# Performance work log

Hardware: AMD Instinct MI355X
Metric: run time of the kernel (lower is better)

The kernel has to match this reference:

```python
import jax, jax.numpy as jnp
import numpy as np

N = 100000   # nodes
K = 32       # fixed neighbor count per node
IN_C = 128
OUT_C = 64


def setup_inputs() -> dict:
    key = jax.random.key(0)
    k1, k2, k3 = jax.random.split(key, 3)
    x = jax.random.normal(k1, (N, IN_C), dtype=jnp.float32)
    nbrs = jax.random.randint(k2, (N, K), 0, N, dtype=jnp.int64)
    # nn.Linear weight [out, in], no bias
    W = jax.random.normal(k3, (OUT_C, IN_C), dtype=jnp.float32) * (1.0 / np.sqrt(IN_C))
    return {"x": x, "nbrs": nbrs, "W": W}


def reference(x, nbrs, W):
    # h = self.w(x): [N, out]
    h = jnp.einsum("ni,oi->no", x, W)
    # gather neighbor features: [N, K, out]
    gathered = h[nbrs]
    # torch.median(dim=0): lower middle element of sorted values (no averaging)
    med_idx = (K - 1) // 2
    out = jnp.sort(gathered, axis=1)[:, med_idx, :]  # [N, out]
    return out
```

## Files before the change

### kernel.cpp

```cpp
#include <hip/hip_runtime.h>
#include <hip/hip_fp16.h>

#define NNODES 100000
#define KNBR 32
#define IN_C 128
#define OUT_C 64

__global__ __launch_bounds__(256) void gemm_h_kernel(
    const float* __restrict__ x, const float* __restrict__ W,
    __half* __restrict__ h)
{
    __shared__ __align__(16) float sx[64 * 68];
    __shared__ __align__(16) float sw[64 * 68];

    const int t = threadIdx.x;
    const int node0 = blockIdx.x * 64;
    const int tx = t & 15;
    const int ty = t >> 4;
    const int kq = t & 15;
    const int sl = t >> 4;

    float acc[4][4];
#pragma unroll
    for (int i = 0; i < 4; ++i)
#pragma unroll
        for (int j = 0; j < 4; ++j) acc[i][j] = 0.f;

    for (int kc = 0; kc < 2; ++kc) {
        const int kbase = kc * 64;
        __syncthreads();
#pragma unroll
        for (int pass = 0; pass < 4; ++pass) {
            const int nl = sl + pass * 16;
            int nn = node0 + nl;
            if (nn > NNODES - 1) nn = NNODES - 1;
            const float4 xv = *(const float4*)(x + nn * IN_C + kbase + 4 * kq);
            sx[(4 * kq + 0) * 68 + nl] = xv.x;
            sx[(4 * kq + 1) * 68 + nl] = xv.y;
            sx[(4 * kq + 2) * 68 + nl] = xv.z;
            sx[(4 * kq + 3) * 68 + nl] = xv.w;
            const float4 wv = *(const float4*)(W + nl * IN_C + kbase + 4 * kq);
            sw[(4 * kq + 0) * 68 + nl] = wv.x;
            sw[(4 * kq + 1) * 68 + nl] = wv.y;
            sw[(4 * kq + 2) * 68 + nl] = wv.z;
            sw[(4 * kq + 3) * 68 + nl] = wv.w;
        }
        __syncthreads();
#pragma unroll 8
        for (int kk = 0; kk < 64; ++kk) {
            const float4 wv = *(const float4*)&sw[kk * 68 + 4 * tx];
            const float4 xv = *(const float4*)&sx[kk * 68 + 4 * ty];
            acc[0][0] += xv.x * wv.x; acc[0][1] += xv.x * wv.y;
            acc[0][2] += xv.x * wv.z; acc[0][3] += xv.x * wv.w;
            acc[1][0] += xv.y * wv.x; acc[1][1] += xv.y * wv.y;
            acc[1][2] += xv.y * wv.z; acc[1][3] += xv.y * wv.w;
            acc[2][0] += xv.z * wv.x; acc[2][1] += xv.z * wv.y;
            acc[2][2] += xv.z * wv.z; acc[2][3] += xv.z * wv.w;
            acc[3][0] += xv.w * wv.x; acc[3][1] += xv.w * wv.y;
            acc[3][2] += xv.w * wv.z; acc[3][3] += xv.w * wv.w;
        }
    }
#pragma unroll
    for (int i = 0; i < 4; ++i) {
        const int node = node0 + 4 * ty + i;
        if (node < NNODES) {
            __half2 p0 = __floats2half2_rn(acc[i][0], acc[i][1]);
            __half2 p1 = __floats2half2_rn(acc[i][2], acc[i][3]);
            uint2 st;
            st.x = *(unsigned int*)&p0;
            st.y = *(unsigned int*)&p1;
            *(uint2*)(h + node * OUT_C + 4 * tx) = st;
        }
    }
}

__device__ __forceinline__ unsigned pk_min(unsigned a, unsigned b) {
    unsigned d;
    asm("v_pk_min_f16 %0, %1, %2" : "=v"(d) : "v"(a), "v"(b));
    return d;
}
__device__ __forceinline__ unsigned pk_max(unsigned a, unsigned b) {
    unsigned d;
    asm("v_pk_max_f16 %0, %1, %2" : "=v"(d) : "v"(a), "v"(b));
    return d;
}
__device__ __forceinline__ void ce(unsigned& a, unsigned& b) {
    const unsigned lo = pk_min(a, b);
    b = pk_max(a, b);
    a = lo;
}

__device__ __forceinline__ void sort16(unsigned* v) {
    constexpr unsigned char net[63][2] = {
        {0,1},{2,3},{4,5},{6,7},{8,9},{10,11},{12,13},{14,15},
        {0,2},{1,3},{4,6},{5,7},{8,10},{9,11},{12,14},{13,15},
        {1,2},{5,6},{9,10},{13,14},
        {0,4},{1,5},{2,6},{3,7},{8,12},{9,13},{10,14},{11,15},
        {2,4},{3,5},{10,12},{11,13},
        {1,2},{3,4},{5,6},{9,10},{11,12},{13,14},
        {0,8},{1,9},{2,10},{3,11},{4,12},{5,13},{6,14},{7,15},
        {4,8},{5,9},{6,10},{7,11},
        {2,4},{3,5},{6,8},{7,9},{10,12},{11,13},
        {1,2},{3,4},{5,6},{7,8},{9,10},{11,12},{13,14}
    };
#pragma unroll
    for (int i = 0; i < 63; ++i) ce(v[net[i][0]], v[net[i][1]]);
}

__device__ __forceinline__ unsigned median32(unsigned* v) {
    sort16(v);
    sort16(v + 16);
    const unsigned* A = v;
    const unsigned* B = v + 16;
    const unsigned e2a = pk_max(pk_max(A[0], B[0]), pk_min(A[8],  B[8]));
    const unsigned o1a = pk_min(pk_max(A[4], B[4]), pk_min(A[12], B[12]));
    const unsigned Ep4 = pk_max(e2a, o1a);
    const unsigned e2b = pk_max(pk_max(A[2], B[2]), pk_min(A[10], B[10]));
    const unsigned o1b = pk_min(pk_max(A[6], B[6]), pk_min(A[14], B[14]));
    const unsigned Op3 = pk_min(e2b, o1b);
    const unsigned E8  = pk_max(Ep4, Op3);
    const unsigned e2c = pk_max(pk_max(A[1], B[1]), pk_min(A[9],  B[9]));
    const unsigned o1c = pk_min(pk_max(A[5], B[5]), pk_min(A[13], B[13]));
    const unsigned Ep4o = pk_max(e2c, o1c);
    const unsigned e2d = pk_max(pk_max(A[3], B[3]), pk_min(A[11], B[11]));
    const unsigned o1d = pk_min(pk_max(A[7], B[7]), pk_min(A[15], B[15]));
    const unsigned Op3o = pk_min(e2d, o1d);
    const unsigned O7  = pk_min(Ep4o, Op3o);
    return pk_min(E8, O7);
}

__global__ __launch_bounds__(256) void median_kernel(
    const __half* __restrict__ h, const int* __restrict__ nbrs,
    float* __restrict__ out)
{
    const int t = threadIdx.x;
    const int li = t & 15;
    const int node = blockIdx.x * 16 + (t >> 4);
    const int ch0 = 4 * li;

    const int ia = nbrs[node * KNBR + li];
    const int ib = nbrs[node * KNBR + 16 + li];

    unsigned a[KNBR];
    unsigned b[KNBR];
#pragma unroll
    for (int k = 0; k < KNBR; ++k) {
        const int row = (k < 16) ? __shfl(ia, k, 16) : __shfl(ib, k - 16, 16);
        const uint2 rv = *(const uint2*)(h + row * OUT_C + ch0);
        a[k] = rv.x;
        b[k] = rv.y;
    }

    const unsigned ma = median32(a);
    const unsigned mb = median32(b);
    const __half2 ha = *(const __half2*)&ma;
    const __half2 hb = *(const __half2*)&mb;

    float4 o;
    o.x = __low2float(ha);
    o.y = __high2float(ha);
    o.z = __low2float(hb);
    o.w = __high2float(hb);
    *(float4*)(out + node * OUT_C + ch0) = o;
}

extern "C" void kernel_launch(void* const* d_in, const int* in_sizes, int n_in,
                              void* d_out, int out_size, void* d_ws, size_t ws_size,
                              hipStream_t stream) {
    (void)in_sizes; (void)n_in; (void)out_size; (void)ws_size;
    const float* x    = (const float*)d_in[0];
    const int*   nbrs = (const int*)d_in[1];
    const float* W    = (const float*)d_in[2];
    float* out = (float*)d_out;
    __half* h  = (__half*)d_ws;

    gemm_h_kernel<<<(NNODES + 63) / 64, 256, 0, stream>>>(x, W, h);
    median_kernel<<<NNODES / 16, 256, 0, stream>>>(h, nbrs, out);
}
```

Measured before the change: 163.3 us.

## Use fp16 MFMA for projection GEMM and nontemporal access in median kernel

Replaces the shared-memory fp32 FMA GEMM with a one-wavefront-per-16-node kernel that converts x and W to fp16 in registers and uses 16x16x32 f16 MFMA instructions, with no LDS staging or barriers. Each block reloads and converts the full W into register fragments. Neighbor indices are loaded and outputs stored with nontemporal hints so streaming data does not displace the gathered h rows in cache. Rounding x and W to fp16 with round-toward-zero before accumulating adds precision loss, and the output stores from the MFMA layout are scalar half writes.

```diff
diff --git a/kernel.cpp b/kernel.cpp
--- a/kernel.cpp
+++ b/kernel.cpp
@@ -5,73 +5,55 @@
 #define KNBR 32
 #define IN_C 128
 #define OUT_C 64
+#define NTILES (NNODES / 16)
 
-__global__ __launch_bounds__(256) void gemm_h_kernel(
+typedef _Float16 half8  __attribute__((ext_vector_type(8)));
+typedef __fp16   fp16x2 __attribute__((ext_vector_type(2)));
+typedef float    f4     __attribute__((ext_vector_type(4)));
+
+union H8 { half8 v; fp16x2 h2[4]; };
+
+__device__ __forceinline__ half8 load_frag_f32(const float* p) {
+    const float4 a = *(const float4*)p;
+    const float4 b = *(const float4*)(p + 4);
+    H8 r;
+    r.h2[0] = __builtin_amdgcn_cvt_pkrtz(a.x, a.y);
+    r.h2[1] = __builtin_amdgcn_cvt_pkrtz(a.z, a.w);
+    r.h2[2] = __builtin_amdgcn_cvt_pkrtz(b.x, b.y);
+    r.h2[3] = __builtin_amdgcn_cvt_pkrtz(b.z, b.w);
+    return r.v;
+}
+
+__global__ __launch_bounds__(64) void gemm_h_kernel(
     const float* __restrict__ x, const float* __restrict__ W,
     __half* __restrict__ h)
 {
-    __shared__ __align__(16) float sx[64 * 68];
-    __shared__ __align__(16) float sw[64 * 68];
+    const int l = threadIdx.x;
+    const int m = l & 15;
+    const int q = l >> 4;
+    const int node0 = blockIdx.x * 16;
 
-    const int t = threadIdx.x;
-    const int node0 = blockIdx.x * 64;
-    const int tx = t & 15;
-    const int ty = t >> 4;
-    const int kq = t & 15;
-    const int sl = t >> 4;
+    half8 wf[4][4];
+#pragma unroll
+    for (int b = 0; b < 4; ++b)
+#pragma unroll
+        for (int kc = 0; kc < 4; ++kc)
+            wf[b][kc] = load_frag_f32(W + (16 * b + m) * IN_C + kc * 32 + 8 * q);
 
-    float acc[4][4];
+    f4 acc[4] = {};
 #pragma unroll
-    for (int i = 0; i < 4; ++i)
+    for (int kc = 0; kc < 4; ++kc) {
+        const half8 af = load_frag_f32(x + (size_t)(node0 + m) * IN_C + kc * 32 + 8 * q);
 #pragma unroll
-        for (int j = 0; j < 4; ++j) acc[i][j] = 0.f;
+        for (int b = 0; b < 4; ++b)
+            acc[b] = __builtin_amdgcn_mfma_f32_16x16x32_f16(af, wf[b][kc], acc[b], 0, 0, 0);
+    }
 
-    for (int kc = 0; kc < 2; ++kc) {
-        const int kbase = kc * 64;
-        __syncthreads();
 #pragma unroll
-        for (int pass = 0; pass < 4; ++pass) {
-            const int nl = sl + pass * 16;
-            int nn = node0 + nl;
-            if (nn > NNODES - 1) nn = NNODES - 1;
-            const float4 xv = *(const float4*)(x + nn * IN_C + kbase + 4 * kq);
-            sx[(4 * kq + 0) * 68 + nl] = xv.x;
-            sx[(4 * kq + 1) * 68 + nl] = xv.y;
-            sx[(4 * kq + 2) * 68 + nl] = xv.z;
-            sx[(4 * kq + 3) * 68 + nl] = xv.w;
-            const float4 wv = *(const float4*)(W + nl * IN_C + kbase + 4 * kq);
-            sw[(4 * kq + 0) * 68 + nl] = wv.x;
-            sw[(4 * kq + 1) * 68 + nl] = wv.y;
-            sw[(4 * kq + 2) * 68 + nl] = wv.z;
-            sw[(4 * kq + 3) * 68 + nl] = wv.w;
-        }
-        __syncthreads();
-#pragma unroll 8
-        for (int kk = 0; kk < 64; ++kk) {
-            const float4 wv = *(const float4*)&sw[kk * 68 + 4 * tx];
-            const float4 xv = *(const float4*)&sx[kk * 68 + 4 * ty];
-            acc[0][0] += xv.x * wv.x; acc[0][1] += xv.x * wv.y;
-            acc[0][2] += xv.x * wv.z; acc[0][3] += xv.x * wv.w;
-            acc[1][0] += xv.y * wv.x; acc[1][1] += xv.y * wv.y;
-            acc[1][2] += xv.y * wv.z; acc[1][3] += xv.y * wv.w;
-            acc[2][0] += xv.z * wv.x; acc[2][1] += xv.z * wv.y;
-            acc[2][2] += xv.z * wv.z; acc[2][3] += xv.z * wv.w;
-            acc[3][0] += xv.w * wv.x; acc[3][1] += xv.w * wv.y;
-            acc[3][2] += xv.w * wv.z; acc[3][3] += xv.w * wv.w;
-        }
-    }
+    for (int b = 0; b < 4; ++b)
 #pragma unroll
-    for (int i = 0; i < 4; ++i) {
-        const int node = node0 + 4 * ty + i;
-        if (node < NNODES) {
-            __half2 p0 = __floats2half2_rn(acc[i][0], acc[i][1]);
-            __half2 p1 = __floats2half2_rn(acc[i][2], acc[i][3]);
-            uint2 st;
-            st.x = *(unsigned int*)&p0;
-            st.y = *(unsigned int*)&p1;
-            *(uint2*)(h + node * OUT_C + 4 * tx) = st;
-        }
-    }
+        for (int r = 0; r < 4; ++r)
+            h[(node0 + 4 * q + r) * OUT_C + 16 * b + m] = __float2half(acc[b][r]);
 }
 
 __device__ __forceinline__ unsigned pk_min(unsigned a, unsigned b) {
@@ -138,8 +120,8 @@
     const int node = blockIdx.x * 16 + (t >> 4);
     const int ch0 = 4 * li;
 
-    const int ia = nbrs[node * KNBR + li];
-    const int ib = nbrs[node * KNBR + 16 + li];
+    const int ia = __builtin_nontemporal_load(nbrs + node * KNBR + li);
+    const int ib = __builtin_nontemporal_load(nbrs + node * KNBR + 16 + li);
 
     unsigned a[KNBR];
     unsigned b[KNBR];
@@ -156,12 +138,12 @@
     const __half2 ha = *(const __half2*)&ma;
     const __half2 hb = *(const __half2*)&mb;
 
-    float4 o;
+    f4 o;
     o.x = __low2float(ha);
     o.y = __high2float(ha);
     o.z = __low2float(hb);
     o.w = __high2float(hb);
-    *(float4*)(out + node * OUT_C + ch0) = o;
+    __builtin_nontemporal_store(o, (f4*)(out + node * OUT_C + ch0));
 }
 
 extern "C" void kernel_launch(void* const* d_in, const int* in_sizes, int n_in,
@@ -174,6 +156,6 @@
     float* out = (float*)d_out;
     __half* h  = (__half*)d_ws;
 
-    gemm_h_kernel<<<(NNODES + 63) / 64, 256, 0, stream>>>(x, W, h);
+    gemm_h_kernel<<<NTILES, 64, 0, stream>>>(x, W, h);
     median_kernel<<<NNODES / 16, 256, 0, stream>>>(h, nbrs, out);
 }
```

New measurement: 163.6 us. About the same (+0.2%).
